# Kernel tuning notes

Measured on AMD Instinct MI355X. Metric: run time of the kernel, lower is better.

## Reference

```python
import math
import jax
import jax.numpy as jnp
import numpy as np

B, S, S_IMG, D, H, MAX_SEQ = 8, 1024, 1, 1024, 16, 1024
HD = D // H


def setup_inputs() -> dict:
    key = jax.random.key(0)
    ks = jax.random.split(key, 8)
    w = 0.02  # GPT-2 init scale keeps softmax well-conditioned
    return {
        "hidden_states": jax.random.normal(ks[0], (B, S, D), jnp.float32),
        "attention_mask": jnp.ones((B, 1, 1, S + S_IMG), jnp.float32),
        "image_hidden_states": jax.random.normal(ks[1], (B, S_IMG, D), jnp.float32),
        "Wc_attn": jax.random.normal(ks[2], (D, 3 * D), jnp.float32) * w,  # Conv1D: x @ W + b
        "bc_attn": jnp.zeros((3 * D,), jnp.float32),
        "Wc_proj": jax.random.normal(ks[3], (D, D), jnp.float32) * w,
        "bc_proj": jnp.zeros((D,), jnp.float32),
        "Wuk": jax.random.normal(ks[4], (D, D), jnp.float32) * w,  # nn.Linear weight: x @ W.T
        "Wuv": jax.random.normal(ks[5], (D, D), jnp.float32) * w,
    }


def _split_heads(x):
    b, s, _ = x.shape
    return x.reshape(b, s, H, HD).transpose(0, 2, 1, 3)  # [B,H,S,hd]


def reference(hidden_states, attention_mask, image_hidden_states,
              Wc_attn, bc_attn, Wc_proj, bc_proj, Wuk, Wuv):
    # c_attn (Conv1D): x @ W + b, then split into q,k,v
    qkv = hidden_states @ Wc_attn + bc_attn
    q, k, v = jnp.split(qkv, 3, axis=-1)
    q, k, v = _split_heads(q), _split_heads(k), _split_heads(v)

    # image KV via bias-free Linear layers, appended to text KV (layer_past=None)
    k_img = _split_heads(image_hidden_states @ Wuk.T)
    v_img = _split_heads(image_hidden_states @ Wuv.T)
    k = jnp.concatenate([k, k_img], axis=2)
    v = jnp.concatenate([v, v_img], axis=2)

    Q, K = q.shape[2], k.shape[2]
    scores = jnp.einsum("bhqd,bhkd->bhqk", q, k) / math.sqrt(HD)

    # causal mask: tril(ones(max_seq_len, max_seq_len+1)) sliced to [Q,K]
    causal = jnp.tril(jnp.ones((MAX_SEQ, MAX_SEQ + 1), bool))[None, None, :Q, :K]
    scores = jnp.where(causal, scores, jnp.float32(-1e9))
    scores = jnp.where(attention_mask == 0, jnp.float32(-1e4), scores)

    p_attn = jax.nn.softmax(scores, axis=-1)  # dropout p=0 -> identity
    x = jnp.einsum("bhqk,bhkd->bhqd", p_attn, v)
    x = x.transpose(0, 2, 1, 3).reshape(hidden_states.shape[0], Q, D)
    return x @ Wc_proj + bc_proj
```

## Files before the change

kernel.cpp:

```cpp
#include <hip/hip_runtime.h>


#define DEVINL __device__ __forceinline__

typedef __attribute__((ext_vector_type(8))) short bf16x8;
typedef __attribute__((ext_vector_type(4))) float f32x4;
typedef __attribute__((ext_vector_type(16))) float f32x16;
typedef __attribute__((ext_vector_type(4))) unsigned int u32x4;

DEVINL unsigned short f2bf(float f) {
  unsigned u = __float_as_uint(f);
  u += 0x7fffu + ((u >> 16) & 1u);
  return (unsigned short)(u >> 16);
}

DEVINL void gload_lds16(const void* g, void* l) {
  __builtin_amdgcn_global_load_lds(
      (const __attribute__((address_space(1))) void*)g,
      (__attribute__((address_space(3))) void*)l, 16, 0, 0);
}

#define BARRIER() asm volatile("s_barrier" ::: "memory")

__global__ void cast_f32_bf16(const float* __restrict__ in,
                              unsigned short* __restrict__ out, int n4) {
  int i = blockIdx.x * blockDim.x + threadIdx.x;
  if (i >= n4) return;
  float4 f = ((const float4*)in)[i];
  uint2 o;
  o.x = (unsigned)f2bf(f.x) | ((unsigned)f2bf(f.y) << 16);
  o.y = (unsigned)f2bf(f.z) | ((unsigned)f2bf(f.w) << 16);
  ((uint2*)out)[i] = o;
}

__global__ void transpose_cast(const float* __restrict__ in,
                               unsigned short* __restrict__ out,
                               int rows, int cols) {
  __shared__ unsigned short tile[32][33];
  int bx = blockIdx.x * 32, by = blockIdx.y * 32;
  int tx = threadIdx.x, ty = threadIdx.y;
#pragma unroll
  for (int i = 0; i < 32; i += 8)
    tile[ty + i][tx] = f2bf(in[(size_t)(by + ty + i) * cols + bx + tx]);
  __syncthreads();
#pragma unroll
  for (int i = 0; i < 32; i += 8)
    out[(size_t)(bx + ty + i) * rows + by + tx] = tile[tx][ty + i];
}

DEVINL void stage_tile(const unsigned short* __restrict__ A,
                       const unsigned short* __restrict__ Bt, int m0, int n0,
                       int kt, int buf, int t, int w, unsigned char* lds) {
  const int base = buf * 24576;
#pragma unroll
  for (int i = 0; i < 2; i++) {
    const int idx = i * 256 + t;
    const int r = idx >> 2, p = idx & 3;
    const int c = p ^ ((r >> 1) & 3);
    gload_lds16(A + (size_t)(m0 + r) * 1024 + kt * 32 + c * 8,
                lds + base + (i * 256 + w * 64) * 16);
  }
#pragma unroll
  for (int i = 0; i < 4; i++) {
    const int idx = i * 256 + t;
    const int r = idx >> 2, p = idx & 3;
    const int c = p ^ ((r >> 1) & 3);
    gload_lds16(Bt + (size_t)(n0 + r) * 1024 + kt * 32 + c * 8,
                lds + base + 8192 + (i * 256 + w * 64) * 16);
  }
}

DEVINL bf16x8 readA2(const unsigned char* lds, int buf, int m, int wr, int lr,
                     int lg) {
  const int row = wr * 64 + m * 16 + lr;
  const int off = (lg ^ ((row >> 1) & 3)) << 4;
  return *(const bf16x8*)(lds + buf * 24576 + row * 64 + off);
}
DEVINL bf16x8 readB2(const unsigned char* lds, int buf, int n, int wc, int lr,
                     int lg) {
  const int row = wc * 128 + n * 16 + lr;
  const int off = (lg ^ ((row >> 1) & 3)) << 4;
  return *(const bf16x8*)(lds + buf * 24576 + 8192 + row * 64 + off);
}

DEVINL void gemm_core(const unsigned short* __restrict__ A,
                      const unsigned short* __restrict__ Bt, int m0, int n0,
                      unsigned char* lds, f32x4 (&acc)[4][8]) {
  const int t = threadIdx.x, w = t >> 6, l = t & 63, lr = l & 15, lg = l >> 4;
  const int wr = w >> 1, wc = w & 1;
  const int NT = 32;

  stage_tile(A, Bt, m0, n0, 0, 0, t, w, lds);
  stage_tile(A, Bt, m0, n0, 1, 1, t, w, lds);
  asm volatile("s_waitcnt vmcnt(6)" ::: "memory");
  __builtin_amdgcn_sched_barrier(0);
  BARRIER();

#pragma unroll 1
  for (int j = 0; j < NT; ++j) {
    const int buf = j % 3;
    if (j + 2 < NT) stage_tile(A, Bt, m0, n0, j + 2, (j + 2) % 3, t, w, lds);
    bf16x8 af[4], bf[8];
#pragma unroll
    for (int m = 0; m < 4; m++) af[m] = readA2(lds, buf, m, wr, lr, lg);
#pragma unroll
    for (int n = 0; n < 8; n++) bf[n] = readB2(lds, buf, n, wc, lr, lg);
    __builtin_amdgcn_s_setprio(1);
#pragma unroll
    for (int m = 0; m < 4; m++)
#pragma unroll
      for (int n = 0; n < 8; n++)
        acc[m][n] = __builtin_amdgcn_mfma_f32_16x16x32_bf16(af[m], bf[n],
                                                            acc[m][n], 0, 0, 0);
    __builtin_amdgcn_s_setprio(0);
    if (j + 1 < NT) {
      if (j + 2 < NT) {
        asm volatile("s_waitcnt vmcnt(6)" ::: "memory");
      } else {
        asm volatile("s_waitcnt vmcnt(0)" ::: "memory");
      }
      __builtin_amdgcn_sched_barrier(0);
      BARRIER();
    }
  }
}

DEVINL void tile_coords(int& m0, int& n0) {
  const int x = blockIdx.x & 7;
  const int local = blockIdx.x >> 3;
  const int mi = local & 7, ni = local >> 3;
  m0 = (x * 8 + mi) * 128;
  n0 = ni * 256;
}

DEVINL int perm16(int x) { return (x & 3) | ((x & 4) << 1) | ((x & 8) >> 1); }

__global__ __launch_bounds__(256, 2) void gemm_qkv(
    const unsigned short* __restrict__ A, const unsigned short* __restrict__ Bt,
    const float* __restrict__ bias, unsigned short* __restrict__ Qb,
    unsigned short* __restrict__ Kb, unsigned short* __restrict__ VTb) {
  __shared__ __align__(16) unsigned char lds[73728];
  f32x4 acc[4][8];
#pragma unroll
  for (int m = 0; m < 4; m++)
#pragma unroll
    for (int n = 0; n < 8; n++)
#pragma unroll
      for (int e = 0; e < 4; e++) acc[m][n][e] = 0.f;
  int m0, n0;
  tile_coords(m0, n0);
  gemm_core(A, Bt, m0, n0, lds, acc);

  const int t = threadIdx.x, w = t >> 6, l = t & 63, lr = l & 15, lg = l >> 4;
  const int wr = w >> 1, wc = w & 1;
  const int region = n0 >> 10;
  const int h0 = (n0 & 1023) >> 6;

  __syncthreads();
  unsigned short* epi = (unsigned short*)lds;
  if (region < 2) {
#pragma unroll
    for (int n = 0; n < 8; n++) {
      const int c = wc * 128 + n * 16 + lr;
      const float bv = bias[n0 + c];
#pragma unroll
      for (int m = 0; m < 4; m++)
#pragma unroll
        for (int e = 0; e < 4; e++) {
          const int r = wr * 64 + m * 16 + lg * 4 + e;
          epi[r * 264 + c] = f2bf(acc[m][n][e] + bv);
        }
    }
  } else {
#pragma unroll
    for (int n = 0; n < 8; n++) {
      const int c = wc * 128 + n * 16 + lr;
      const float bv = bias[n0 + c];
#pragma unroll
      for (int m = 0; m < 4; m++)
#pragma unroll
        for (int e = 0; e < 4; e++) {
          const int rp = wr * 64 + m * 16 + perm16(lg * 4 + e);
          epi[c * 136 + rp] = f2bf(acc[m][n][e] + bv);
        }
    }
  }
  __syncthreads();

  if (region < 2) {
    const int row = t & 127, half = t >> 7;
    unsigned short* dbuf = (region == 0) ? Qb : Kb;
    const int sg = m0 + row, b = sg >> 10, si = sg & 1023;
#pragma unroll
    for (int hh = 0; hh < 2; hh++) {
      const int head = h0 + half * 2 + hh;
      const unsigned short* src = epi + row * 264 + half * 128 + hh * 64;
      unsigned short* dst = dbuf + (((size_t)b * 16 + head) * 1024 + si) * 64;
#pragma unroll
      for (int i = 0; i < 8; i++)
        ((u32x4*)dst)[i] = *(const u32x4*)(src + i * 8);
    }
  } else {
    const int c = t;
    const int head = h0 + (c >> 6), hd = c & 63;
    const int b = m0 >> 10, s0 = m0 & 1023;
    const unsigned short* src = epi + c * 136;
    unsigned short* dst = VTb + (((size_t)b * 16 + head) * 64 + hd) * 1024 + s0;
#pragma unroll
    for (int i = 0; i < 16; i++)
      ((u32x4*)dst)[i] = *(const u32x4*)(src + i * 8);
  }
}

__global__ __launch_bounds__(256, 2) void gemm_proj(
    const unsigned short* __restrict__ A, const unsigned short* __restrict__ Bt,
    const float* __restrict__ bias, float* __restrict__ out) {
  __shared__ __align__(16) unsigned char lds[73728];
  f32x4 acc[4][8];
#pragma unroll
  for (int m = 0; m < 4; m++)
#pragma unroll
    for (int n = 0; n < 8; n++)
#pragma unroll
      for (int e = 0; e < 4; e++) acc[m][n][e] = 0.f;
  int m0, n0;
  tile_coords(m0, n0);
  gemm_core(A, Bt, m0, n0, lds, acc);
  const int t = threadIdx.x, w = t >> 6, l = t & 63, lr = l & 15, lg = l >> 4;
  const int wr = w >> 1, wc = w & 1;
#pragma unroll
  for (int n = 0; n < 8; n++) {
    const int col = n0 + wc * 128 + n * 16 + lr;
    const float bv = bias[col];
#pragma unroll
    for (int m = 0; m < 4; m++)
#pragma unroll
      for (int e = 0; e < 4; e++) {
        const int row = m0 + wr * 64 + m * 16 + lg * 4 + e;
        out[(size_t)row * 1024 + col] = acc[m][n][e] + bv;
      }
  }
}

DEVINL void load_kv(int j0, const unsigned short* kbase,
                    const unsigned short* vb0, const unsigned short* vb1,
                    bf16x8 (&kf)[4], bf16x8 (&vf)[4]) {
#pragma unroll
  for (int ks = 0; ks < 4; ks++)
    kf[ks] = *(const bf16x8*)(kbase + (size_t)j0 * 64 + ks * 16);
  vf[0] = *(const bf16x8*)(vb0 + j0);
  vf[1] = *(const bf16x8*)(vb0 + j0 + 16);
  vf[2] = *(const bf16x8*)(vb1 + j0);
  vf[3] = *(const bf16x8*)(vb1 + j0 + 16);
}

template <bool DIAG>
DEVINL void attn_compute(int r, int hi, const bf16x8 (&kf)[4],
                         const bf16x8 (&vf)[4], const bf16x8 (&qf)[4],
                         f32x16& o0, f32x16& o1, float& lsum) {
  f32x16 s;
#pragma unroll
  for (int e = 0; e < 16; e++) s[e] = 0.f;
  __builtin_amdgcn_s_setprio(1);
#pragma unroll
  for (int ks = 0; ks < 4; ks++)
    s = __builtin_amdgcn_mfma_f32_32x32x16_bf16(kf[ks], qf[ks], s, 0, 0, 0);
  __builtin_amdgcn_s_setprio(0);
  float p[16];
  float ls = 0.f;
#pragma unroll
  for (int e = 0; e < 16; e++) {
    float pv = __expf(s[e] * 0.125f);
    if (DIAG) {
      const int jr = (e & 3) + 8 * (e >> 2) + 4 * hi;
      if (jr > r) pv = 0.f;
    }
    p[e] = pv;
    ls += pv;
  }
  lsum += ls;
  unsigned wv[8];
#pragma unroll
  for (int i = 0; i < 8; i++)
    asm("v_cvt_pk_bf16_f32 %0, %1, %2"
        : "=v"(wv[i]) : "v"(p[2 * i]), "v"(p[2 * i + 1]));
  u32x4 w0, w1;
  w0[0] = wv[0]; w0[1] = wv[1]; w0[2] = wv[2]; w0[3] = wv[3];
  w1[0] = wv[4]; w1[1] = wv[5]; w1[2] = wv[6]; w1[3] = wv[7];
  bf16x8 pa0 = __builtin_bit_cast(bf16x8, w0);
  bf16x8 pa1 = __builtin_bit_cast(bf16x8, w1);
  __builtin_amdgcn_s_setprio(1);
  o0 = __builtin_amdgcn_mfma_f32_32x32x16_bf16(pa0, vf[0], o0, 0, 0, 0);
  o0 = __builtin_amdgcn_mfma_f32_32x32x16_bf16(pa1, vf[1], o0, 0, 0, 0);
  o1 = __builtin_amdgcn_mfma_f32_32x32x16_bf16(pa0, vf[2], o1, 0, 0, 0);
  o1 = __builtin_amdgcn_mfma_f32_32x32x16_bf16(pa1, vf[3], o1, 0, 0, 0);
  __builtin_amdgcn_s_setprio(0);
}

__global__ __launch_bounds__(256) void attn_kernel(
    const unsigned short* __restrict__ Qb, const unsigned short* __restrict__ Kb,
    const unsigned short* __restrict__ VTb, unsigned short* __restrict__ Xb) {
  __shared__ float lsums[4][32];
  const int bh = blockIdx.x;
  const int t = threadIdx.x, w = t >> 6, l = t & 63;
  const int r = l & 31, hi = l >> 5;
  const int q0 = blockIdx.y * 128 + w * 32;

  bf16x8 qf[4];
  const unsigned short* qp = Qb + ((size_t)bh * 1024 + q0 + r) * 64 + hi * 8;
#pragma unroll
  for (int ks = 0; ks < 4; ks++) qf[ks] = *(const bf16x8*)(qp + ks * 16);

  f32x16 o0, o1;
#pragma unroll
  for (int e = 0; e < 16; e++) { o0[e] = 0.f; o1[e] = 0.f; }
  float lsum = 0.f;

  const unsigned short* kbase = Kb + ((size_t)bh * 1024 + r) * 64 + hi * 8;
  const unsigned short* vb0 = VTb + ((size_t)(bh * 64 + r)) * 1024 + hi * 8;
  const unsigned short* vb1 = vb0 + (size_t)32 * 1024;
  const int nt = (q0 >> 5) + 1;

  bf16x8 kf[4], vf[4];
  load_kv(0, kbase, vb0, vb1, kf, vf);
#pragma unroll 1
  for (int tt = 0; tt < nt - 1; ++tt) {
    bf16x8 kn[4], vn[4];
    load_kv((tt + 1) * 32, kbase, vb0, vb1, kn, vn);
    attn_compute<false>(r, hi, kf, vf, qf, o0, o1, lsum);
#pragma unroll
    for (int i = 0; i < 4; i++) { kf[i] = kn[i]; vf[i] = vn[i]; }
  }
  attn_compute<true>(r, hi, kf, vf, qf, o0, o1, lsum);

  float ltot = lsum + __shfl_xor(lsum, 32, 64);
  if (l < 32) lsums[w][l] = ltot;

  const int bb = bh >> 4, h = bh & 15;
#pragma unroll
  for (int e = 0; e < 16; e++) {
    const int rw = (e & 3) + 8 * (e >> 2) + 4 * hi;
    const float inv = 1.0f / lsums[w][rw];
    unsigned short* xp = Xb + ((size_t)bb * 1024 + q0 + rw) * 1024 + h * 64 + r;
    xp[0]  = f2bf(o0[e] * inv);
    xp[32] = f2bf(o1[e] * inv);
  }
}

extern "C" void kernel_launch(void* const* d_in, const int* in_sizes, int n_in,
                              void* d_out, int out_size, void* d_ws,
                              size_t ws_size, hipStream_t stream) {
  const float* hidden = (const float*)d_in[0];
  const float* Wattn = (const float*)d_in[3];
  const float* battn = (const float*)d_in[4];
  const float* Wproj = (const float*)d_in[5];
  const float* bproj = (const float*)d_in[6];

  unsigned short* hB  = (unsigned short*)d_ws;
  unsigned short* WaT = hB + (size_t)8192 * 1024;
  unsigned short* WpT = WaT + (size_t)3072 * 1024;
  unsigned short* Qb  = WpT + (size_t)1024 * 1024;
  unsigned short* Kb  = Qb + (size_t)8192 * 1024;
  unsigned short* VTb = Kb + (size_t)8192 * 1024;
  unsigned short* Xb  = hB;

  cast_f32_bf16<<<8192, 256, 0, stream>>>(hidden, hB, 2097152);
  transpose_cast<<<dim3(96, 32), dim3(32, 8), 0, stream>>>(Wattn, WaT, 1024, 3072);
  transpose_cast<<<dim3(32, 32), dim3(32, 8), 0, stream>>>(Wproj, WpT, 1024, 1024);
  gemm_qkv<<<768, 256, 0, stream>>>(hB, WaT, battn, Qb, Kb, VTb);
  attn_kernel<<<dim3(128, 8), 256, 0, stream>>>(Qb, Kb, VTb, Xb);
  gemm_proj<<<256, 256, 0, stream>>>(Xb, WpT, bproj, (float*)d_out);
}
```

Before: 183.7 us.

## Process two 32-row query groups per wave to reuse K/V loads

Each attention wave now handles 64 query rows, as two 32-row groups sharing each loaded K/V tile, and the grid is halved in y. This halves the global K/V load traffic per query row and gives more MFMA work per load to hide latency. In exchange it doubles accumulator registers, which may reduce occupancy, halves block count, and makes causal work across waves less even.

After: 158.7 us. 13.6% less time.

```diff
diff --git a/kernel.cpp b/kernel.cpp
--- a/kernel.cpp
+++ b/kernel.cpp
@@ -255,9 +255,9 @@
 }
 
 template <bool DIAG>
-DEVINL void attn_compute(int r, int hi, const bf16x8 (&kf)[4],
-                         const bf16x8 (&vf)[4], const bf16x8 (&qf)[4],
-                         f32x16& o0, f32x16& o1, float& lsum) {
+DEVINL void attn_group(int r, int hi, const bf16x8 (&kf)[4],
+                       const bf16x8 (&vf)[4], const bf16x8 (&qf)[4],
+                       f32x16& o0, f32x16& o1, float& lsum) {
   f32x16 s;
 #pragma unroll
   for (int e = 0; e < 16; e++) s[e] = 0.f;
@@ -300,50 +300,70 @@
 __global__ __launch_bounds__(256) void attn_kernel(
     const unsigned short* __restrict__ Qb, const unsigned short* __restrict__ Kb,
     const unsigned short* __restrict__ VTb, unsigned short* __restrict__ Xb) {
-  __shared__ float lsums[4][32];
+  __shared__ float lsums[4][2][32];
   const int bh = blockIdx.x;
   const int t = threadIdx.x, w = t >> 6, l = t & 63;
   const int r = l & 31, hi = l >> 5;
-  const int q0 = blockIdx.y * 128 + w * 32;
-
-  bf16x8 qf[4];
-  const unsigned short* qp = Qb + ((size_t)bh * 1024 + q0 + r) * 64 + hi * 8;
-#pragma unroll
-  for (int ks = 0; ks < 4; ks++) qf[ks] = *(const bf16x8*)(qp + ks * 16);
-
-  f32x16 o0, o1;
-#pragma unroll
-  for (int e = 0; e < 16; e++) { o0[e] = 0.f; o1[e] = 0.f; }
-  float lsum = 0.f;
+  const int qbase = blockIdx.y * 256 + w * 64;
+
+  bf16x8 qfA[4], qfB[4];
+  const unsigned short* qp = Qb + ((size_t)bh * 1024 + qbase + r) * 64 + hi * 8;
+#pragma unroll
+  for (int ks = 0; ks < 4; ks++) {
+    qfA[ks] = *(const bf16x8*)(qp + ks * 16);
+    qfB[ks] = *(const bf16x8*)(qp + 32 * 64 + ks * 16);
+  }
+
+  f32x16 oA0, oA1, oB0, oB1;
+#pragma unroll
+  for (int e = 0; e < 16; e++) {
+    oA0[e] = 0.f; oA1[e] = 0.f; oB0[e] = 0.f; oB1[e] = 0.f;
+  }
+  float lsumA = 0.f, lsumB = 0.f;
 
   const unsigned short* kbase = Kb + ((size_t)bh * 1024 + r) * 64 + hi * 8;
   const unsigned short* vb0 = VTb + ((size_t)(bh * 64 + r)) * 1024 + hi * 8;
   const unsigned short* vb1 = vb0 + (size_t)32 * 1024;
-  const int nt = (q0 >> 5) + 1;
+  const int nd = qbase >> 5;
 
   bf16x8 kf[4], vf[4];
   load_kv(0, kbase, vb0, vb1, kf, vf);
 #pragma unroll 1
-  for (int tt = 0; tt < nt - 1; ++tt) {
+  for (int tt = 0; tt < nd; ++tt) {
     bf16x8 kn[4], vn[4];
     load_kv((tt + 1) * 32, kbase, vb0, vb1, kn, vn);
-    attn_compute<false>(r, hi, kf, vf, qf, o0, o1, lsum);
+    attn_group<false>(r, hi, kf, vf, qfA, oA0, oA1, lsumA);
+    attn_group<false>(r, hi, kf, vf, qfB, oB0, oB1, lsumB);
 #pragma unroll
     for (int i = 0; i < 4; i++) { kf[i] = kn[i]; vf[i] = vn[i]; }
   }
-  attn_compute<true>(r, hi, kf, vf, qf, o0, o1, lsum);
-
-  float ltot = lsum + __shfl_xor(lsum, 32, 64);
-  if (l < 32) lsums[w][l] = ltot;
+  {
+    bf16x8 kn[4], vn[4];
+    load_kv((nd + 1) * 32, kbase, vb0, vb1, kn, vn);
+    attn_group<true>(r, hi, kf, vf, qfA, oA0, oA1, lsumA);
+    attn_group<false>(r, hi, kf, vf, qfB, oB0, oB1, lsumB);
+#pragma unroll
+    for (int i = 0; i < 4; i++) { kf[i] = kn[i]; vf[i] = vn[i]; }
+  }
+  attn_group<true>(r, hi, kf, vf, qfB, oB0, oB1, lsumB);
+
+  float ltotA = lsumA + __shfl_xor(lsumA, 32, 64);
+  float ltotB = lsumB + __shfl_xor(lsumB, 32, 64);
+  if (l < 32) { lsums[w][0][l] = ltotA; lsums[w][1][l] = ltotB; }
 
   const int bb = bh >> 4, h = bh & 15;
 #pragma unroll
   for (int e = 0; e < 16; e++) {
     const int rw = (e & 3) + 8 * (e >> 2) + 4 * hi;
-    const float inv = 1.0f / lsums[w][rw];
-    unsigned short* xp = Xb + ((size_t)bb * 1024 + q0 + rw) * 1024 + h * 64 + r;
-    xp[0]  = f2bf(o0[e] * inv);
-    xp[32] = f2bf(o1[e] * inv);
+    const float invA = 1.0f / lsums[w][0][rw];
+    const float invB = 1.0f / lsums[w][1][rw];
+    unsigned short* xpA =
+        Xb + ((size_t)bb * 1024 + qbase + rw) * 1024 + h * 64 + r;
+    unsigned short* xpB = xpA + (size_t)32 * 1024;
+    xpA[0]  = f2bf(oA0[e] * invA);
+    xpA[32] = f2bf(oA1[e] * invA);
+    xpB[0]  = f2bf(oB0[e] * invB);
+    xpB[32] = f2bf(oB1[e] * invB);
   }
 }
 
@@ -368,6 +388,6 @@
   transpose_cast<<<dim3(96, 32), dim3(32, 8), 0, stream>>>(Wattn, WaT, 1024, 3072);
   transpose_cast<<<dim3(32, 32), dim3(32, 8), 0, stream>>>(Wproj, WpT, 1024, 1024);
   gemm_qkv<<<768, 256, 0, stream>>>(hB, WaT, battn, Qb, Kb, VTb);
-  attn_kernel<<<dim3(128, 8), 256, 0, stream>>>(Qb, Kb, VTb, Xb);
+  attn_kernel<<<dim3(128, 4), 256, 0, stream>>>(Qb, Kb, VTb, Xb);
   gemm_proj<<<256, 256, 0, stream>>>(Xb, WpT, bproj, (float*)d_out);
 }
```
